# Optimization experiments

Measured on AMD Instinct MI355X. Metric: run time of the kernel, lower is better.

Reference implementation:

```python
import jax, jax.numpy as jnp
import numpy as np


def _shift(a, sx, sy):
    """Return a[..., i+sx, j+sy] with zero fill outside the grid."""
    pad = [(0, 0)] * (a.ndim - 2) + [(1, 1), (1, 1)]
    p = jnp.pad(a, pad)
    Nx, Ny = a.shape[-2], a.shape[-1]
    return p[..., 1 + sx:1 + sx + Nx, 1 + sy:1 + sy + Ny]


def _fp2d_step(A, D, f, dt, ensure_non_negative_f=True):
    """Finite-difference Fokker-Planck step in grid units (dx = 1):
    df/dt = -d_x(Ax f) - d_y(Ay f) + 1/2 d_xx(Dxx f) + 1/2 d_yy(Dyy f) + d_xy(Dxy f)
    Central differences, zero (vacuum) boundary conditions.
    A: (2, Nx, Ny), D: (3, Nx, Ny) [Dxx, Dyy, Dxy], f: (B, Nx, Ny).
    """
    Fx = A[0] * f
    Fy = A[1] * f
    Gxx = D[0] * f
    Gyy = D[1] * f
    Gxy = D[2] * f

    # first derivatives (central)
    dFx = 0.5 * (_shift(Fx, 1, 0) - _shift(Fx, -1, 0))
    dFy = 0.5 * (_shift(Fy, 0, 1) - _shift(Fy, 0, -1))
    # second derivatives
    d2Gxx = _shift(Gxx, 1, 0) - 2.0 * Gxx + _shift(Gxx, -1, 0)
    d2Gyy = _shift(Gyy, 0, 1) - 2.0 * Gyy + _shift(Gyy, 0, -1)
    # mixed derivative
    d2Gxy = 0.25 * (_shift(Gxy, 1, 1) - _shift(Gxy, 1, -1)
                    - _shift(Gxy, -1, 1) + _shift(Gxy, -1, -1))

    rhs = -(dFx + dFy) + 0.5 * (d2Gxx + d2Gyy) + d2Gxy
    f_new = f + dt * rhs
    if ensure_non_negative_f:
        f_new = jnp.maximum(f_new, 0.0)
    return f_new


def setup_inputs() -> dict:
    key = jax.random.key(0)
    kf, kA, kD = jax.random.split(key, 3)
    B, Nx, Ny = 128, 512, 512
    f = jax.random.uniform(kf, (B, Nx, Ny), dtype=jnp.float32)
    A = 0.1 * jax.random.normal(kA, (2, Nx, Ny), dtype=jnp.float32)
    D = 0.1 * jax.random.uniform(kD, (3, Nx, Ny), dtype=jnp.float32)
    dt = jnp.float32(0.1)
    return {"f": f, "A": A, "D": D, "dt": dt}


def reference(f, A, D, dt):
    # ensure_non_negative_D=False, guard_cells=False per init_kwargs
    return _fp2d_step(A=A, D=D, f=f, dt=dt, ensure_non_negative_f=True)
```

## Files before the change

kernel.cpp:

```cpp
#include <hip/hip_runtime.h>


namespace {

constexpr int N   = 512;
constexpr long NN = (long)N * N;
constexpr int SPR = N / 4;

__device__ __forceinline__ float4 ld4(const float* __restrict__ p) {
    return *reinterpret_cast<const float4*>(p);
}

struct W6 { float v[6]; };

__device__ __forceinline__ W6 load6(const float* __restrict__ row, int j0,
                                    int jl, int jr, float mL, float mR) {
    W6 w;
    const float4 c = ld4(row + j0);
    w.v[0] = row[jl] * mL;
    w.v[1] = c.x; w.v[2] = c.y; w.v[3] = c.z; w.v[4] = c.w;
    w.v[5] = row[jr] * mR;
    return w;
}

__device__ __forceinline__ void unpack4(float* d, float4 t) {
    d[0] = t.x; d[1] = t.y; d[2] = t.z; d[3] = t.w;
}

}

extern "C" __global__ __launch_bounds__(256) void fp2d_step(
    const float* __restrict__ f,
    const float* __restrict__ A,
    const float* __restrict__ D,
    const float* __restrict__ dtp,
    float* __restrict__ out)
{
    int bid = (int)blockIdx.x;
    {
        const int nwg = (int)gridDim.x;
        const int nx = 8;
        const int chunk = nwg / nx;
        if (chunk * nx == nwg) bid = (bid % nx) * chunk + (bid / nx);
    }

    const long tid = (long)bid * 256 + threadIdx.x;
    const int  s   = (int)(tid % SPR);
    const int  i   = (int)((tid / SPR) % N);
    const int  b   = (int)(tid / ((long)SPR * N));
    const int  j0  = s * 4;

    const float dt = dtp[0];

    const int   im = (i > 0)     ? i - 1 : 0;
    const int   ip = (i < N - 1) ? i + 1 : N - 1;
    const float mm = (i > 0)     ? 1.f : 0.f;
    const float mp = (i < N - 1) ? 1.f : 0.f;
    const int   jl = (j0 > 0)      ? j0 - 1 : 0;
    const int   jr = (j0 + 4 < N)  ? j0 + 4 : N - 1;
    const float mL = (j0 > 0)      ? 1.f : 0.f;
    const float mR = (j0 + 4 < N)  ? 1.f : 0.f;

    const float* fb  = f + b * NN;
    W6 fm = load6(fb + (long)im * N, j0, jl, jr, mL, mR);
    W6 fc = load6(fb + (long)i  * N, j0, jl, jr, mL, mR);
    W6 fp = load6(fb + (long)ip * N, j0, jl, jr, mL, mR);
#pragma unroll
    for (int k = 0; k < 6; ++k) { fm.v[k] *= mm; fp.v[k] *= mp; }

    const float* A0 = A;
    const float* A1 = A + NN;
    const float* D0 = D;
    const float* D1 = D + NN;
    const float* D2 = D + 2 * NN;

    float a0m[4], a0p[4], d0m[4], d0c[4], d0p[4];
    unpack4(a0m, ld4(A0 + (long)im * N + j0));
    unpack4(a0p, ld4(A0 + (long)ip * N + j0));
    unpack4(d0m, ld4(D0 + (long)im * N + j0));
    unpack4(d0c, ld4(D0 + (long)i  * N + j0));
    unpack4(d0p, ld4(D0 + (long)ip * N + j0));
    const W6 a1  = load6(A1 + (long)i  * N, j0, jl, jr, mL, mR);
    const W6 d1  = load6(D1 + (long)i  * N, j0, jl, jr, mL, mR);
    const W6 d2m = load6(D2 + (long)im * N, j0, jl, jr, mL, mR);
    const W6 d2p = load6(D2 + (long)ip * N, j0, jl, jr, mL, mR);

    float r[4];
#pragma unroll
    for (int k = 0; k < 4; ++k) {
        const float fL  = fc.v[k], fC  = fc.v[k + 1], fR  = fc.v[k + 2];
        const float fmL = fm.v[k], fmC = fm.v[k + 1], fmR = fm.v[k + 2];
        const float fpL = fp.v[k], fpC = fp.v[k + 1], fpR = fp.v[k + 2];

        float rhs;
        rhs  = -0.5f * (a0p[k] * fpC - a0m[k] * fmC);
        rhs -= 0.5f * (a1.v[k + 2] * fR - a1.v[k] * fL);
        rhs += 0.5f * (d0p[k] * fpC - 2.f * d0c[k] * fC + d0m[k] * fmC);
        rhs += 0.5f * (d1.v[k + 2] * fR - 2.f * d1.v[k + 1] * fC + d1.v[k] * fL);
        rhs += 0.25f * (d2p.v[k + 2] * fpR - d2p.v[k] * fpL
                      - d2m.v[k + 2] * fmR + d2m.v[k] * fmL);

        const float val = fC + dt * rhs;
        r[k] = val > 0.f ? val : 0.f;
    }

    float4 o;
    o.x = r[0]; o.y = r[1]; o.z = r[2]; o.w = r[3];
    *reinterpret_cast<float4*>(out + b * NN + (long)i * N + j0) = o;
}

extern "C" void kernel_launch(void* const* d_in, const int* in_sizes, int n_in,
                              void* d_out, int out_size, void* d_ws, size_t ws_size,
                              hipStream_t stream) {
    const float* f   = (const float*)d_in[0];
    const float* A   = (const float*)d_in[1];
    const float* D   = (const float*)d_in[2];
    const float* dtp = (const float*)d_in[3];
    float* out = (float*)d_out;

    const int B = in_sizes[0] / (int)NN;
    const long threads = (long)B * N * SPR;
    const unsigned grid = (unsigned)(threads / 256);

    hipLaunchKernelGGL(fp2d_step, dim3(grid), dim3(256), 0, stream,
                       f, A, D, dtp, out);
}
```

Before: 371.7 us.

## March each thread down T rows with register-rotated stencil rows

Measured after the change: 329.5 us. 1.13x faster.

```diff
diff --git a/kernel.cpp b/kernel.cpp
--- a/kernel.cpp
+++ b/kernel.cpp
@@ -6,6 +6,10 @@
 constexpr int N   = 512;
 constexpr long NN = (long)N * N;
 constexpr int SPR = N / 4;
+constexpr int T   = 8;
+constexpr int BANDS = N / (2 * T);
+
+typedef float f4 __attribute__((ext_vector_type(4)));
 
 __device__ __forceinline__ float4 ld4(const float* __restrict__ p) {
     return *reinterpret_cast<const float4*>(p);
@@ -23,8 +27,11 @@
     return w;
 }
 
-__device__ __forceinline__ void unpack4(float* d, float4 t) {
-    d[0] = t.x; d[1] = t.y; d[2] = t.z; d[3] = t.w;
+struct C4 { float v[4]; };
+__device__ __forceinline__ C4 ldc4(const float* __restrict__ p) {
+    const float4 t = ld4(p);
+    C4 c; c.v[0] = t.x; c.v[1] = t.y; c.v[2] = t.z; c.v[3] = t.w;
+    return c;
 }
 
 }
@@ -36,77 +43,89 @@
     const float* __restrict__ dtp,
     float* __restrict__ out)
 {
-    int bid = (int)blockIdx.x;
-    {
-        const int nwg = (int)gridDim.x;
-        const int nx = 8;
-        const int chunk = nwg / nx;
-        if (chunk * nx == nwg) bid = (bid % nx) * chunk + (bid / nx);
-    }
+    const int blk  = (int)blockIdx.x;
+    const int band = blk >> 7;
+    const int b    = blk & 127;
 
-    const long tid = (long)bid * 256 + threadIdx.x;
-    const int  s   = (int)(tid % SPR);
-    const int  i   = (int)((tid / SPR) % N);
-    const int  b   = (int)(tid / ((long)SPR * N));
-    const int  j0  = s * 4;
+    const int s  = (int)threadIdx.x & (SPR - 1);
+    const int rg = (int)threadIdx.x >> 7;
+    const int i0 = (band * 2 + rg) * T;
+    const int j0 = s * 4;
 
     const float dt = dtp[0];
 
-    const int   im = (i > 0)     ? i - 1 : 0;
-    const int   ip = (i < N - 1) ? i + 1 : N - 1;
-    const float mm = (i > 0)     ? 1.f : 0.f;
-    const float mp = (i < N - 1) ? 1.f : 0.f;
-    const int   jl = (j0 > 0)      ? j0 - 1 : 0;
-    const int   jr = (j0 + 4 < N)  ? j0 + 4 : N - 1;
-    const float mL = (j0 > 0)      ? 1.f : 0.f;
-    const float mR = (j0 + 4 < N)  ? 1.f : 0.f;
+    const int   jl = (j0 > 0)     ? j0 - 1 : 0;
+    const int   jr = (j0 + 4 < N) ? j0 + 4 : N - 1;
+    const float mL = (j0 > 0)     ? 1.f : 0.f;
+    const float mR = (j0 + 4 < N) ? 1.f : 0.f;
 
-    const float* fb  = f + b * NN;
-    W6 fm = load6(fb + (long)im * N, j0, jl, jr, mL, mR);
-    W6 fc = load6(fb + (long)i  * N, j0, jl, jr, mL, mR);
-    W6 fp = load6(fb + (long)ip * N, j0, jl, jr, mL, mR);
-#pragma unroll
-    for (int k = 0; k < 6; ++k) { fm.v[k] *= mm; fp.v[k] *= mp; }
-
+    const float* fb = f + (long)b * NN;
     const float* A0 = A;
     const float* A1 = A + NN;
     const float* D0 = D;
     const float* D1 = D + NN;
     const float* D2 = D + 2 * NN;
 
-    float a0m[4], a0p[4], d0m[4], d0c[4], d0p[4];
-    unpack4(a0m, ld4(A0 + (long)im * N + j0));
-    unpack4(a0p, ld4(A0 + (long)ip * N + j0));
-    unpack4(d0m, ld4(D0 + (long)im * N + j0));
-    unpack4(d0c, ld4(D0 + (long)i  * N + j0));
-    unpack4(d0p, ld4(D0 + (long)ip * N + j0));
-    const W6 a1  = load6(A1 + (long)i  * N, j0, jl, jr, mL, mR);
-    const W6 d1  = load6(D1 + (long)i  * N, j0, jl, jr, mL, mR);
-    const W6 d2m = load6(D2 + (long)im * N, j0, jl, jr, mL, mR);
-    const W6 d2p = load6(D2 + (long)ip * N, j0, jl, jr, mL, mR);
+    const int   im0 = (i0 > 0) ? i0 - 1 : 0;
+    const float mm0 = (i0 > 0) ? 1.f : 0.f;
 
-    float r[4];
+    W6 fm = load6(fb + (long)im0 * N, j0, jl, jr, mL, mR);
 #pragma unroll
-    for (int k = 0; k < 4; ++k) {
-        const float fL  = fc.v[k], fC  = fc.v[k + 1], fR  = fc.v[k + 2];
-        const float fmL = fm.v[k], fmC = fm.v[k + 1], fmR = fm.v[k + 2];
-        const float fpL = fp.v[k], fpC = fp.v[k + 1], fpR = fp.v[k + 2];
+    for (int k = 0; k < 6; ++k) fm.v[k] *= mm0;
+    W6 fc = load6(fb + (long)i0 * N, j0, jl, jr, mL, mR);
 
-        float rhs;
-        rhs  = -0.5f * (a0p[k] * fpC - a0m[k] * fmC);
-        rhs -= 0.5f * (a1.v[k + 2] * fR - a1.v[k] * fL);
-        rhs += 0.5f * (d0p[k] * fpC - 2.f * d0c[k] * fC + d0m[k] * fmC);
-        rhs += 0.5f * (d1.v[k + 2] * fR - 2.f * d1.v[k + 1] * fC + d1.v[k] * fL);
-        rhs += 0.25f * (d2p.v[k + 2] * fpR - d2p.v[k] * fpL
-                      - d2m.v[k + 2] * fmR + d2m.v[k] * fmL);
+    C4 a0m = ldc4(A0 + (long)im0 * N + j0);
+    C4 a0c = ldc4(A0 + (long)i0  * N + j0);
+    C4 d0m = ldc4(D0 + (long)im0 * N + j0);
+    C4 d0c = ldc4(D0 + (long)i0  * N + j0);
+    W6 d2m = load6(D2 + (long)im0 * N, j0, jl, jr, mL, mR);
+    W6 d2c = load6(D2 + (long)i0  * N, j0, jl, jr, mL, mR);
 
-        const float val = fC + dt * rhs;
-        r[k] = val > 0.f ? val : 0.f;
+    float* ob = out + (long)b * NN + (long)i0 * N + j0;
+
+#pragma unroll
+    for (int t = 0; t < T; ++t) {
+        const int   i   = i0 + t;
+        const int   ipr = (i + 1 < N) ? i + 1 : N - 1;
+        const float mp  = (i + 1 < N) ? 1.f : 0.f;
+
+        W6 fp = load6(fb + (long)ipr * N, j0, jl, jr, mL, mR);
+#pragma unroll
+        for (int k = 0; k < 6; ++k) fp.v[k] *= mp;
+
+        const C4 a0p = ldc4(A0 + (long)ipr * N + j0);
+        const C4 d0p = ldc4(D0 + (long)ipr * N + j0);
+        const W6 d2p = load6(D2 + (long)ipr * N, j0, jl, jr, mL, mR);
+        const W6 a1  = load6(A1 + (long)i   * N, j0, jl, jr, mL, mR);
+        const W6 d1  = load6(D1 + (long)i   * N, j0, jl, jr, mL, mR);
+
+        f4 o;
+#pragma unroll
+        for (int k = 0; k < 4; ++k) {
+            const float fL  = fc.v[k], fC  = fc.v[k + 1], fR  = fc.v[k + 2];
+            const float fmL = fm.v[k], fmC = fm.v[k + 1], fmR = fm.v[k + 2];
+            const float fpL = fp.v[k], fpC = fp.v[k + 1], fpR = fp.v[k + 2];
+
+            float rhs;
+            rhs  = -0.5f * (a0p.v[k] * fpC - a0m.v[k] * fmC);
+            rhs -= 0.5f * (a1.v[k + 2] * fR - a1.v[k] * fL);
+            rhs += 0.5f * (d0p.v[k] * fpC - 2.f * d0c.v[k] * fC + d0m.v[k] * fmC);
+            rhs += 0.5f * (d1.v[k + 2] * fR - 2.f * d1.v[k + 1] * fC + d1.v[k] * fL);
+            rhs += 0.25f * (d2p.v[k + 2] * fpR - d2p.v[k] * fpL
+                          - d2m.v[k + 2] * fmR + d2m.v[k] * fmL);
+
+            const float val = fC + dt * rhs;
+            o[k] = val > 0.f ? val : 0.f;
+        }
+
+        __builtin_nontemporal_store(o, reinterpret_cast<f4*>(ob));
+        ob += N;
+
+        fm  = fc;  fc  = fp;
+        a0m = a0c; a0c = a0p;
+        d0m = d0c; d0c = d0p;
+        d2m = d2c; d2c = d2p;
     }
-
-    float4 o;
-    o.x = r[0]; o.y = r[1]; o.z = r[2]; o.w = r[3];
-    *reinterpret_cast<float4*>(out + b * NN + (long)i * N + j0) = o;
 }
 
 extern "C" void kernel_launch(void* const* d_in, const int* in_sizes, int n_in,
@@ -119,8 +138,7 @@
     float* out = (float*)d_out;
 
     const int B = in_sizes[0] / (int)NN;
-    const long threads = (long)B * N * SPR;
-    const unsigned grid = (unsigned)(threads / 256);
+    const unsigned grid = (unsigned)(BANDS * B);
 
     hipLaunchKernelGGL(fp2d_step, dim3(grid), dim3(256), 0, stream,
                        f, A, D, dtp, out);
```
